# Performance work log

Hardware: AMD Instinct MI355X
Metric: run time of the kernel (lower is better)

## Reference

```python
import jax, jax.numpy as jnp
import numpy as np

MIN_SIGMA = 1e-3  # min_sigma from __init__
EPS = 1e-16


def rbf_kernel(A, B, sigma):
    """A: (bs, n, d), B: (m, d) -> K: (bs, n, m) with K = exp(-||a-b||^2 / (2 sigma^2))."""
    s = jnp.maximum(sigma, MIN_SIGMA)
    a2 = jnp.sum(A * A, axis=-1, keepdims=True)              # (bs, n, 1)
    b2 = jnp.sum(B * B, axis=-1)                             # (m,)
    d2 = a2 + b2[None, None, :] - 2.0 * jnp.einsum('bnd,md->bnm', A, B)
    d2 = jnp.maximum(d2, 0.0)
    return jnp.exp(-d2 / (2.0 * s * s))


def setup_inputs() -> dict:
    key = jax.random.key(0)
    k1, k2, k3 = jax.random.split(key, 3)
    BS, N, DX, DY, M = 256, 128, 32, 10, 2048  # batch, items(bag), dim_x, dim_y, n_comp
    inputs = jax.random.normal(k1, (BS, N, DX), dtype=jnp.float32)
    c_x = jax.random.normal(k2, (M, DX), dtype=jnp.float32)
    c_y = jax.random.uniform(k3, (M, DY), dtype=jnp.float32)
    comp_w = jnp.full((M,), 1.0 / M, dtype=jnp.float32)
    # sigma chosen ~ sqrt(dim_x) so RBF values don't underflow for Gaussian inputs
    sigma = jnp.float32(8.0)
    return {"inputs": inputs, "sigma": sigma, "c_x": c_x, "c_y": c_y, "comp_w": comp_w}


def reference(inputs, sigma, c_x, c_y, comp_w):
    bs, n, _ = inputs.shape
    # comp2dm: uniform bag weights w, components = inputs
    w = jnp.full((bs, n), 1.0 / n, dtype=inputs.dtype)       # (bs, n)
    # KQMUnit: kernel measurement
    K = rbf_kernel(inputs, c_x, sigma)                        # (bs, n, n_comp)
    out_w = jnp.einsum('bn,bnm->bm', w, comp_w[None, None, :] * (K * K))  # (bs, n_comp)
    out_w_sum = jnp.sum(out_w, axis=-1, keepdims=True)
    y_w = out_w / jnp.where(out_w_sum == 0, EPS, out_w_sum)   # normalized mixture weights
    # dm2comp + row-normalize components (batch-independent c_y)
    y_v = c_y / jnp.linalg.norm(c_y, axis=-1, keepdims=True)  # (n_comp, dim_y)
    # probs = einsum('...j,...ji->...i', y_w, y_v**2)
    probs = jnp.einsum('bm,md->bd', y_w, y_v * y_v)           # (bs, dim_y)
    return probs
```

## Files before the change

### kernel.cpp

```cpp
#include <hip/hip_runtime.h>
#include <hip/hip_bf16.h>

#define BS     256
#define N_BAG  128
#define DXD    32
#define DYD    10
#define M_COMP 2048
#define CHUNKS 8

typedef __attribute__((ext_vector_type(8))) short short8v;
typedef __attribute__((ext_vector_type(4))) float f32x4;

static __device__ __forceinline__ unsigned int pkbf(float a, float b) {
    unsigned short ha = __bfloat16_as_ushort(__float2bfloat16(a));
    unsigned short hb = __bfloat16_as_ushort(__float2bfloat16(b));
    return (unsigned int)ha | ((unsigned int)hb << 16);
}
static __device__ __forceinline__ float fast_exp2(float x) {
#if __has_builtin(__builtin_amdgcn_exp2f)
    return __builtin_amdgcn_exp2f(x);
#else
    return __expf(x * 0.6931471805599453f);
#endif
}

__global__ __launch_bounds__(256, 8) void main_kernel(
    const float* __restrict__ X,
    const float* __restrict__ sig_p,
    const float* __restrict__ c_x,
    const float* __restrict__ c_y,
    const float* __restrict__ comp_w,
    float* __restrict__ part)
{
    __shared__ short8v Af[8][64];
    __shared__ float   a2part[N_BAG][4];
    __shared__ float   a2c[N_BAG];
    __shared__ float   ow_s[2][256];
    __shared__ float   red[4][12];

    const int tid   = threadIdx.x;
    const int bid   = blockIdx.x;
    const int b     = bid >> 3;
    const int chunk = bid & 7;

    const float sgm = fmaxf(sig_p[0], 1e-3f);
    const float c2  = -1.4426950408889634f / (sgm * sgm);
    const float sA  = -2.0f * c2;

#pragma unroll
    for (int k = 0; k < 2; ++k) {
        const int u = tid + 256 * k;
        const int n = u >> 2, g4 = u & 3;
        const float4* Xr = (const float4*)(X + ((size_t)(b * N_BAG + n) * DXD + 8 * g4));
        float4 v0 = Xr[0], v1 = Xr[1];
        float s = 0.f;
        s = fmaf(v0.x, v0.x, s); s = fmaf(v0.y, v0.y, s);
        s = fmaf(v0.z, v0.z, s); s = fmaf(v0.w, v0.w, s);
        s = fmaf(v1.x, v1.x, s); s = fmaf(v1.y, v1.y, s);
        s = fmaf(v1.z, v1.z, s); s = fmaf(v1.w, v1.w, s);
        union { unsigned int u4[4]; short8v s8; } cv;
        cv.u4[0] = pkbf(sA * v0.x, sA * v0.y); cv.u4[1] = pkbf(sA * v0.z, sA * v0.w);
        cv.u4[2] = pkbf(sA * v1.x, sA * v1.y); cv.u4[3] = pkbf(sA * v1.z, sA * v1.w);
        Af[n >> 4][g4 * 16 + (n & 15)] = cv.s8;
        a2part[n][g4] = s;
    }
    __syncthreads();
    if (tid < N_BAG)
        a2c[tid] = c2 * (a2part[tid][0] + a2part[tid][1] +
                         a2part[tid][2] + a2part[tid][3]);
    __syncthreads();

    const int lane = tid & 63, wv = tid >> 6;
    const int half = wv & 1, wp = wv >> 1;
    const int r = lane & 15, gq = lane >> 4, rowg = gq * 4;

    short8v Xf[4];
    f32x4   s4[4];
#pragma unroll
    for (int j = 0; j < 4; ++j) {
        Xf[j] = Af[half * 4 + j][lane];
        s4[j] = *(const f32x4*)&a2c[(half * 4 + j) * 16 + rowg];
    }

    const int mt_base = chunk * 16 + wp * 8;
#pragma unroll
    for (int i = 0; i < 8; ++i) {
        const int m = (mt_base + i) * 16 + r;
        const float4* cp4 = (const float4*)(c_x + (size_t)m * DXD + 8 * gq);
        float4 p0 = cp4[0], p1 = cp4[1];
        union { unsigned int u4[4]; short8v s8; } bc;
        bc.u4[0] = pkbf(p0.x, p0.y); bc.u4[1] = pkbf(p0.z, p0.w);
        bc.u4[2] = pkbf(p1.x, p1.y); bc.u4[3] = pkbf(p1.z, p1.w);
        float s = 0.f;
        s = fmaf(p0.x, p0.x, s); s = fmaf(p0.y, p0.y, s);
        s = fmaf(p0.z, p0.z, s); s = fmaf(p0.w, p0.w, s);
        s = fmaf(p1.x, p1.x, s); s = fmaf(p1.y, p1.y, s);
        s = fmaf(p1.z, p1.z, s); s = fmaf(p1.w, p1.w, s);
        s += __shfl_xor(s, 16, 64);
        s += __shfl_xor(s, 32, 64);
        const float cbv = c2 * s;

        float cs0 = 0.f, cs1 = 0.f;
#pragma unroll
        for (int j = 0; j < 4; ++j) {
            f32x4 seed = s4[j] + cbv;
            f32x4 acc  = __builtin_amdgcn_mfma_f32_16x16x32_bf16(Xf[j], bc.s8, seed, 0, 0, 0);
            cs0 += fast_exp2(acc[0]); cs1 += fast_exp2(acc[1]);
            cs0 += fast_exp2(acc[2]); cs1 += fast_exp2(acc[3]);
        }
        float csum = cs0 + cs1;
        csum += __shfl_xor(csum, 16, 64);
        csum += __shfl_xor(csum, 32, 64);
        if (lane < 16) ow_s[half][wp * 128 + i * 16 + r] = csum;
    }
    __syncthreads();

    {
        const int m = chunk * 256 + tid;
        const float w = (ow_s[0][tid] + ow_s[1][tid]) * comp_w[m] * (1.0f / N_BAG);
        const float2* cyp = (const float2*)(c_y + (size_t)m * DYD);
        float2 y0 = cyp[0], y1 = cyp[1], y2 = cyp[2], y3 = cyp[3], y4 = cyp[4];
        float cy[DYD] = {y0.x, y0.y, y1.x, y1.y, y2.x, y2.y, y3.x, y3.y, y4.x, y4.y};
        float ny = 0.f;
#pragma unroll
        for (int d = 0; d < DYD; ++d) ny = fmaf(cy[d], cy[d], ny);
        const float yw = w * __builtin_amdgcn_rcpf(ny);
        float vals[DYD + 1];
        vals[0] = w;
#pragma unroll
        for (int d = 0; d < DYD; ++d) vals[1 + d] = yw * cy[d] * cy[d];

#pragma unroll
        for (int v = 0; v <= DYD; ++v) {
            float x = vals[v];
#pragma unroll
            for (int off = 32; off > 0; off >>= 1) x += __shfl_down(x, off, 64);
            if (lane == 0) red[wv][v] = x;
        }
        __syncthreads();
        if (tid <= DYD)
            part[(size_t)bid * 16 + tid] = red[0][tid] + red[1][tid] + red[2][tid] + red[3][tid];
    }
}

__global__ __launch_bounds__(1024) void combine_kernel(const float* __restrict__ part,
                                                       float* __restrict__ out) {
    const int t = threadIdx.x;
    const int b = t >> 2, q = t & 3;
    float s[DYD + 1];
#pragma unroll
    for (int v = 0; v <= DYD; ++v) s[v] = 0.f;
#pragma unroll
    for (int c = 0; c < 2; ++c) {
        const float* p = part + (size_t)(b * 8 + q + 4 * c) * 16;
#pragma unroll
        for (int v = 0; v <= DYD; ++v) s[v] += p[v];
    }
#pragma unroll
    for (int v = 0; v <= DYD; ++v) {
        s[v] += __shfl_xor(s[v], 1, 64);
        s[v] += __shfl_xor(s[v], 2, 64);
    }
    if (q == 0) {
        float d = s[0];
        d = (d == 0.f) ? 1e-16f : d;
        const float inv = 1.0f / d;
#pragma unroll
        for (int dd = 0; dd < DYD; ++dd)
            out[(size_t)b * DYD + dd] = s[1 + dd] * inv;
    }
}

extern "C" void kernel_launch(void* const* d_in, const int* in_sizes, int n_in,
                              void* d_out, int out_size, void* d_ws, size_t ws_size,
                              hipStream_t stream) {
    const float* X      = (const float*)d_in[0];
    const float* sigma  = (const float*)d_in[1];
    const float* c_x    = (const float*)d_in[2];
    const float* c_y    = (const float*)d_in[3];
    const float* comp_w = (const float*)d_in[4];
    float*       out    = (float*)d_out;

    float* part = (float*)d_ws;

    main_kernel<<<BS * CHUNKS, 256, 0, stream>>>(X, sigma, c_x, c_y, comp_w, part);
    combine_kernel<<<1, 1024, 0, stream>>>(part, out);
}
```

Measured before the change: 31.33 us.

## Use 1024-thread blocks covering half the components, precompute center norms in LDS

Each block now handles one batch row and 1024 of the 2048 components using 16 waves, instead of 256-thread blocks over 256-component chunks. The squared norms of the centers are computed once per block into shared memory, replacing the per-tile FMA-and-shuffle recomputation. The exp accumulation is split across four accumulators, and the combine kernel shrinks to two partials per batch. The trade-off is fewer, larger blocks (512 in total) and a launch-bounds hint of 1024 threads with 8 blocks, which may squeeze register allocation and reduce latency hiding.

New measurement: 35.05 us. 11.9% more time.

```diff
diff --git a/kernel.cpp b/kernel.cpp
--- a/kernel.cpp
+++ b/kernel.cpp
@@ -6,7 +6,6 @@
 #define DXD    32
 #define DYD    10
 #define M_COMP 2048
-#define CHUNKS 8
 
 typedef __attribute__((ext_vector_type(8))) short short8v;
 typedef __attribute__((ext_vector_type(4))) float f32x4;
@@ -24,7 +23,7 @@
 #endif
 }
 
-__global__ __launch_bounds__(256, 8) void main_kernel(
+__global__ __launch_bounds__(1024, 8) void main_kernel(
     const float* __restrict__ X,
     const float* __restrict__ sig_p,
     const float* __restrict__ c_x,
@@ -35,22 +34,20 @@
     __shared__ short8v Af[8][64];
     __shared__ float   a2part[N_BAG][4];
     __shared__ float   a2c[N_BAG];
-    __shared__ float   ow_s[2][256];
-    __shared__ float   red[4][12];
+    __shared__ float   b2c[1024];
+    __shared__ float   ow_s[2][1024];
+    __shared__ float   red[16][12];
 
     const int tid   = threadIdx.x;
-    const int bid   = blockIdx.x;
-    const int b     = bid >> 3;
-    const int chunk = bid & 7;
+    const int b     = blockIdx.x >> 1;
+    const int m0    = (blockIdx.x & 1) * 1024;
 
     const float sgm = fmaxf(sig_p[0], 1e-3f);
     const float c2  = -1.4426950408889634f / (sgm * sgm);
     const float sA  = -2.0f * c2;
 
-#pragma unroll
-    for (int k = 0; k < 2; ++k) {
-        const int u = tid + 256 * k;
-        const int n = u >> 2, g4 = u & 3;
+    if (tid < 512) {
+        const int n = tid >> 2, g4 = tid & 3;
         const float4* Xr = (const float4*)(X + ((size_t)(b * N_BAG + n) * DXD + 8 * g4));
         float4 v0 = Xr[0], v1 = Xr[1];
         float s = 0.f;
@@ -63,6 +60,17 @@
         cv.u4[2] = pkbf(sA * v1.x, sA * v1.y); cv.u4[3] = pkbf(sA * v1.z, sA * v1.w);
         Af[n >> 4][g4 * 16 + (n & 15)] = cv.s8;
         a2part[n][g4] = s;
+    }
+    {
+        const float4* cp = (const float4*)(c_x + (size_t)(m0 + tid) * DXD);
+        float s = 0.f;
+#pragma unroll
+        for (int j = 0; j < 8; ++j) {
+            float4 v = cp[j];
+            s = fmaf(v.x, v.x, s); s = fmaf(v.y, v.y, s);
+            s = fmaf(v.z, v.z, s); s = fmaf(v.w, v.w, s);
+        }
+        b2c[tid] = c2 * s;
     }
     __syncthreads();
     if (tid < N_BAG)
@@ -82,41 +90,33 @@
         s4[j] = *(const f32x4*)&a2c[(half * 4 + j) * 16 + rowg];
     }
 
-    const int mt_base = chunk * 16 + wp * 8;
-#pragma unroll
+#pragma unroll 2
     for (int i = 0; i < 8; ++i) {
-        const int m = (mt_base + i) * 16 + r;
-        const float4* cp4 = (const float4*)(c_x + (size_t)m * DXD + 8 * gq);
+        const int ml = (wp * 8 + i) * 16 + r;
+        const float4* cp4 = (const float4*)(c_x + (size_t)(m0 + ml) * DXD + 8 * gq);
         float4 p0 = cp4[0], p1 = cp4[1];
         union { unsigned int u4[4]; short8v s8; } bc;
         bc.u4[0] = pkbf(p0.x, p0.y); bc.u4[1] = pkbf(p0.z, p0.w);
         bc.u4[2] = pkbf(p1.x, p1.y); bc.u4[3] = pkbf(p1.z, p1.w);
-        float s = 0.f;
-        s = fmaf(p0.x, p0.x, s); s = fmaf(p0.y, p0.y, s);
-        s = fmaf(p0.z, p0.z, s); s = fmaf(p0.w, p0.w, s);
-        s = fmaf(p1.x, p1.x, s); s = fmaf(p1.y, p1.y, s);
-        s = fmaf(p1.z, p1.z, s); s = fmaf(p1.w, p1.w, s);
-        s += __shfl_xor(s, 16, 64);
-        s += __shfl_xor(s, 32, 64);
-        const float cbv = c2 * s;
+        const float cbv = b2c[ml];
 
-        float cs0 = 0.f, cs1 = 0.f;
+        float cs0 = 0.f, cs1 = 0.f, cs2 = 0.f, cs3 = 0.f;
 #pragma unroll
         for (int j = 0; j < 4; ++j) {
             f32x4 seed = s4[j] + cbv;
             f32x4 acc  = __builtin_amdgcn_mfma_f32_16x16x32_bf16(Xf[j], bc.s8, seed, 0, 0, 0);
             cs0 += fast_exp2(acc[0]); cs1 += fast_exp2(acc[1]);
-            cs0 += fast_exp2(acc[2]); cs1 += fast_exp2(acc[3]);
+            cs2 += fast_exp2(acc[2]); cs3 += fast_exp2(acc[3]);
         }
-        float csum = cs0 + cs1;
+        float csum = (cs0 + cs1) + (cs2 + cs3);
         csum += __shfl_xor(csum, 16, 64);
         csum += __shfl_xor(csum, 32, 64);
-        if (lane < 16) ow_s[half][wp * 128 + i * 16 + r] = csum;
+        if (lane < 16) ow_s[half][ml] = csum;
     }
     __syncthreads();
 
     {
-        const int m = chunk * 256 + tid;
+        const int m = m0 + tid;
         const float w = (ow_s[0][tid] + ow_s[1][tid]) * comp_w[m] * (1.0f / N_BAG);
         const float2* cyp = (const float2*)(c_y + (size_t)m * DYD);
         float2 y0 = cyp[0], y1 = cyp[1], y2 = cyp[2], y3 = cyp[3], y4 = cyp[4];
@@ -138,37 +138,26 @@
             if (lane == 0) red[wv][v] = x;
         }
         __syncthreads();
-        if (tid <= DYD)
-            part[(size_t)bid * 16 + tid] = red[0][tid] + red[1][tid] + red[2][tid] + red[3][tid];
+        if (tid <= DYD) {
+            float s = 0.f;
+#pragma unroll
+            for (int w16 = 0; w16 < 16; ++w16) s += red[w16][tid];
+            part[(size_t)blockIdx.x * 16 + tid] = s;
+        }
     }
 }
 
-__global__ __launch_bounds__(1024) void combine_kernel(const float* __restrict__ part,
-                                                       float* __restrict__ out) {
-    const int t = threadIdx.x;
-    const int b = t >> 2, q = t & 3;
-    float s[DYD + 1];
+__global__ __launch_bounds__(256) void combine_kernel(const float* __restrict__ part,
+                                                      float* __restrict__ out) {
+    const int b = threadIdx.x;
+    const float* p0 = part + (size_t)(2 * b) * 16;
+    const float* p1 = part + (size_t)(2 * b + 1) * 16;
+    float d = p0[0] + p1[0];
+    d = (d == 0.f) ? 1e-16f : d;
+    const float inv = 1.0f / d;
 #pragma unroll
-    for (int v = 0; v <= DYD; ++v) s[v] = 0.f;
-#pragma unroll
-    for (int c = 0; c < 2; ++c) {
-        const float* p = part + (size_t)(b * 8 + q + 4 * c) * 16;
-#pragma unroll
-        for (int v = 0; v <= DYD; ++v) s[v] += p[v];
-    }
-#pragma unroll
-    for (int v = 0; v <= DYD; ++v) {
-        s[v] += __shfl_xor(s[v], 1, 64);
-        s[v] += __shfl_xor(s[v], 2, 64);
-    }
-    if (q == 0) {
-        float d = s[0];
-        d = (d == 0.f) ? 1e-16f : d;
-        const float inv = 1.0f / d;
-#pragma unroll
-        for (int dd = 0; dd < DYD; ++dd)
-            out[(size_t)b * DYD + dd] = s[1 + dd] * inv;
-    }
+    for (int dd = 0; dd < DYD; ++dd)
+        out[(size_t)b * DYD + dd] = (p0[1 + dd] + p1[1 + dd]) * inv;
 }
 
 extern "C" void kernel_launch(void* const* d_in, const int* in_sizes, int n_in,
@@ -183,6 +172,6 @@
 
     float* part = (float*)d_ws;
 
-    main_kernel<<<BS * CHUNKS, 256, 0, stream>>>(X, sigma, c_x, c_y, comp_w, part);
-    combine_kernel<<<1, 1024, 0, stream>>>(part, out);
+    main_kernel<<<BS * 2, 1024, 0, stream>>>(X, sigma, c_x, c_y, comp_w, part);
+    combine_kernel<<<1, 256, 0, stream>>>(part, out);
 }
```
